# Kernel tuning notes

Hardware: AMD Instinct MI355X
Metric: run time of the kernel (lower is better)

The kernel has to match this reference:

```python
import jax, jax.numpy as jnp
import numpy as np

SELECTOR = jnp.array([29, 49, 79])
N_FINAL = 6
N_EM_ITERS = 10
LOG_2PI = float(np.log(2.0 * np.pi))


def _logdet2(c):
    # log determinant of trailing 2x2 matrices
    return jnp.log(c[..., 0, 0] * c[..., 1, 1] - c[..., 0, 1] * c[..., 1, 0])


def _inv2(c):
    # analytic inverse of trailing 2x2 matrices
    det = c[..., 0, 0] * c[..., 1, 1] - c[..., 0, 1] * c[..., 1, 0]
    inv = jnp.stack([
        jnp.stack([c[..., 1, 1], -c[..., 0, 1]], axis=-1),
        jnp.stack([-c[..., 1, 0], c[..., 0, 0]], axis=-1),
    ], axis=-2)
    return inv / det[..., None, None]


def _initial_state(probas, trajectories):
    B, M = probas.shape
    tsel = trajectories[:, :, SELECTOR, :]                       # [B,M,3,2]
    dots = jnp.einsum('bmtd,bntd->btmn', tsel, tsel)             # [B,3,M,M]
    d1 = jnp.einsum('bmtd,bmtd->btm', tsel, tsel)                # [B,3,M]
    R = jnp.sqrt(d1[:, :, :, None] + d1[:, :, None, :] - 2.0 * dots)
    thr = jnp.quantile(R[:, -1].reshape(B, -1), 0.15, axis=-1)[:, None, None, None]
    adj = (R <= thr).astype(probas.dtype).prod(axis=1)           # [B,M,M]
    worked = jnp.ones((B, M), dtype=probas.dtype)
    bidx = jnp.arange(B)
    idxs = []
    for _ in range(N_FINAL):
        score = (adj * probas[:, None, :]).sum(axis=2) * worked  # [B,M]
        amax = jnp.argmax(score, axis=-1)                        # [B]
        worked = worked * (1.0 - adj[bidx, amax])
        idxs.append(amax)
    return jnp.stack(idxs, axis=1)                               # [B,6]


def _coefficients(cov6, trajectories, traj6, probas6):
    cov6_sel = cov6[:, :, SELECTOR]                              # [B,6,3,2,2]
    prec = _inv2(cov6_sel)                                       # [B,6,3,2,2]
    diff = traj6[:, :, SELECTOR][:, :, None] - trajectories[:, :, SELECTOR][:, None]  # [B,6,M,3,2]
    qform = jnp.einsum('bnmti,bntij,bnmtj->bnmt', diff, prec, diff)
    logdet = _logdet2(cov6_sel)[:, :, None, :]                   # [B,6,1,3]
    pM = jnp.exp((-LOG_2PI - 0.5 * logdet - 0.5 * qform).sum(axis=-1)) + 1e-8  # [B,6,M]
    num = pM * probas6[:, :, None]
    return num / (num.sum(axis=1, keepdims=True) + 1e-8)


def _forward(non_normalized_probas, trajectories, covariance_matrices):
    B = trajectories.shape[0]
    probas = jax.nn.softmax(non_normalized_probas, axis=-1)
    idx = jax.lax.stop_gradient(_initial_state(probas, trajectories))  # [B,6]
    b = jnp.arange(B)[:, None]
    traj6 = trajectories[b, idx]                                 # [B,6,T,2]
    probas6 = jax.nn.softmax(jnp.take_along_axis(non_normalized_probas, idx, axis=1), axis=-1)
    cov6 = covariance_matrices[b, idx]                           # [B,6,T,2,2]
    for _ in range(N_EM_ITERS):
        pM = jax.lax.stop_gradient(_coefficients(cov6, trajectories, traj6, probas6))
        P = probas[:, None, :] * pM                              # [B,6,M]
        probas6 = P.sum(axis=-1)                                 # [B,6]
        traj6 = jnp.einsum('bnm,bmtd->bntd', P, trajectories) / probas6[:, :, None, None]
        diff = traj6[:, :, None] - trajectories[:, None]         # [B,6,M,T,2]
        cov6 = (jnp.einsum('bnm,bmtij->bntij', P, covariance_matrices)
                + jnp.einsum('bnm,bnmti,bnmtj->bntij', P, diff, diff)) / probas6[:, :, None, None, None]
    return probas6, traj6, cov6


def setup_inputs() -> dict:
    key = jax.random.key(0)
    k1, k2, k3 = jax.random.split(key, 3)
    B, M, T = 256, 48, 80
    logits = jax.random.normal(k1, (B, M), dtype=jnp.float32)
    trajectories = jax.random.normal(k2, (B, M, T, 2), dtype=jnp.float32)
    A = 0.3 * jax.random.normal(k3, (B, M, T, 2, 2), dtype=jnp.float32)
    cov = A @ jnp.swapaxes(A, -1, -2) + 0.5 * jnp.eye(2, dtype=jnp.float32)
    return {'non_normalized_probas': logits, 'trajectories': trajectories,
            'covariance_matrices': cov}


def reference(non_normalized_probas, trajectories, covariance_matrices):
    return _forward(non_normalized_probas, trajectories, covariance_matrices)
```

## Files before the change

### kernel.cpp

```cpp
#include <hip/hip_runtime.h>
#include <math.h>

#define BATCH 256
#define M 48
#define T 80
#define NF 6
#define EMIT 10
#define MM (M*M)
#define KPW 9
#define LOG2PI 1.8378770664093453f

typedef unsigned int u32;
typedef unsigned long long u64;

#define WGSYNC()     __asm__ __volatile__("s_waitcnt lgkmcnt(0)\ns_barrier" ::: "memory")
#define WGSYNC_ALL() __asm__ __volatile__("s_waitcnt vmcnt(0) lgkmcnt(0)\ns_barrier" ::: "memory")

__global__ __launch_bounds__(256, 1)
void em_kernel(const float* __restrict__ g_logits,
               const float* __restrict__ g_traj,
               const float* __restrict__ g_cov,
               float* __restrict__ g_out)
{
    const int b = blockIdx.x;
    const int tid = threadIdx.x;
    const int lane = tid & 63;
    const int wv = tid >> 6;
    const int SEL[3] = {29, 49, 79};

    __shared__ __align__(16) float s_txy[M*T*2];
    __shared__ __align__(16) float s_cv4[M*T*4];
    __shared__ float s_adj[MM];
    __shared__ float s_logits[M];
    __shared__ float s_probas[M];
    __shared__ float s_tsel[M*6];
    __shared__ float s_d1[M*3];
    __shared__ __align__(16) float s_csel[M*3*4];
    __shared__ __align__(16) float s_Pm[M*8];
    __shared__ float s_t6sel[2][NF*6];
    __shared__ float s_probas6[2][NF];
    __shared__ float s_prec[2][NF*3*3];
    __shared__ float s_ld[2][NF*3];
    __shared__ int   s_idx[8];
    __shared__ __align__(16) u32 s_hist[4][4][256];
    __shared__ u32 s_statc[4], s_statm[4];

    const float* traj_b = g_traj + (size_t)b*(M*T*2);
    const float* cov_b  = g_cov  + (size_t)b*(M*T*4);

    float myLogit = -1e30f;
    if (lane < M) myLogit = g_logits[b*M + lane];
    float selx[3], sely[3], cc0[3], cc1[3], cc2[3];
    #pragma unroll
    for (int r = 0; r < 3; ++r) {
        int i = lane + r*64;
        if (i < M*3) {
            int m = i/3, tt = i - (i/3)*3;
            float2 xy = ((const float2*)traj_b)[m*T + SEL[tt]];
            float4 cv = ((const float4*)cov_b)[m*T + SEL[tt]];
            selx[r]=xy.x; sely[r]=xy.y; cc0[r]=cv.x; cc1[r]=cv.y; cc2[r]=cv.w;
        }
    }

    __builtin_amdgcn_sched_barrier(0);
    {
        const char* gt = (const char*)traj_b + lane*16;
        char* lt = (char*)s_txy;
        #pragma unroll 2
        for (int k = wv; k < 30; k += 4)
            __builtin_amdgcn_global_load_lds(
                (const __attribute__((address_space(1))) u32*)(gt + k*1024),
                (__attribute__((address_space(3))) u32*)(lt + k*1024), 16, 0, 0);
        const char* gc = (const char*)cov_b + lane*16;
        char* lc = (char*)s_cv4;
        #pragma unroll 2
        for (int k = wv; k < 60; k += 4)
            __builtin_amdgcn_global_load_lds(
                (const __attribute__((address_space(1))) u32*)(gc + k*1024),
                (__attribute__((address_space(3))) u32*)(lc + k*1024), 16, 0, 0);
    }
    __builtin_amdgcn_sched_barrier(0);

    {
        uint4* hz = (uint4*)&s_hist[wv][0][0];
        #pragma unroll
        for (int k = 0; k < 4; ++k) hz[lane + k*64] = make_uint4(0,0,0,0);
    }

    if (lane < M) s_logits[lane] = myLogit;
    #pragma unroll
    for (int r = 0; r < 3; ++r) {
        int i = lane + r*64;
        if (i < M*3) {
            int m = i/3, tt = i - (i/3)*3;
            s_tsel[m*6+tt*2+0] = selx[r];
            s_tsel[m*6+tt*2+1] = sely[r];
            s_d1[i] = selx[r]*selx[r] + sely[r]*sely[r];
            s_csel[i*4+0]=cc0[r]; s_csel[i*4+1]=cc1[r]; s_csel[i*4+2]=cc2[r]; s_csel[i*4+3]=0.f;
        }
    }

    float mx = myLogit;
    #pragma unroll
    for (int off = 32; off; off >>= 1) mx = fmaxf(mx, __shfl_xor(mx, off));
    float pe = (lane < M) ? __expf(myLogit - mx) : 0.f;
    float psum = pe;
    #pragma unroll
    for (int off = 32; off; off >>= 1) psum += __shfl_xor(psum, off);
    const float proba = pe / psum;
    if (lane < M) s_probas[lane] = proba;

    u32 key[KPW];
    {
        u32* h0 = &s_hist[wv][0][0];
        #pragma unroll
        for (int j = 0; j < KPW; ++j) {
            int e = lane + (wv*KPW + j)*64;
            int m = e/M, n = e - (e/M)*M;
            float dot = s_tsel[m*6+4]*s_tsel[n*6+4] + s_tsel[m*6+5]*s_tsel[n*6+5];
            float v = s_d1[m*3+2] + s_d1[n*3+2] - 2.0f*dot;
            key[j] = __float_as_uint(fmaxf(v, 0.0f));
            atomicAdd(&h0[key[j] >> 24], 1u);
        }
    }

    int target = 345;
    u32 prefix = 0u, pmask = 0u;
    #pragma unroll 1
    for (int r = 0; r < 4; ++r) {
        const int shift = 24 - 8*r;
        if (r) {
            u32* hr = &s_hist[wv][r][0];
            #pragma unroll
            for (int j = 0; j < KPW; ++j) {
                if ((key[j] & pmask) == prefix)
                    atomicAdd(&hr[(key[j] >> shift) & 255u], 1u);
            }
        }
        WGSYNC();
        uint4 h0 = ((const uint4*)&s_hist[0][r][0])[lane];
        uint4 h1 = ((const uint4*)&s_hist[1][r][0])[lane];
        uint4 h2 = ((const uint4*)&s_hist[2][r][0])[lane];
        uint4 h3 = ((const uint4*)&s_hist[3][r][0])[lane];
        uint4 hv = make_uint4(h0.x+h1.x+h2.x+h3.x, h0.y+h1.y+h2.y+h3.y,
                              h0.z+h1.z+h2.z+h3.z, h0.w+h1.w+h2.w+h3.w);
        u32 s4 = hv.x + hv.y + hv.z + hv.w;
        u32 cum = s4;
        #pragma unroll
        for (int off = 1; off < 64; off <<= 1) {
            u32 u = __shfl_up(cum, off);
            if (lane >= off) cum += u;
        }
        u64 bmask = __ballot(cum > (u32)target);
        int g = __builtin_ctzll(bmask);
        int dig = 0; u32 binstart = 0;
        if (lane == g) {
            u32 exc = cum - s4;
            int bi2 = lane*4;
            if (exc + hv.x > (u32)target)      { dig = bi2;   binstart = exc; }
            else { exc += hv.x;
                if (exc + hv.y > (u32)target)  { dig = bi2+1; binstart = exc; }
                else { exc += hv.y;
                    if (exc + hv.z > (u32)target) { dig = bi2+2; binstart = exc; }
                    else { exc += hv.z;            dig = bi2+3; binstart = exc; } } }
        }
        dig = __shfl(dig, g);
        binstart = (u32)__shfl((int)binstart, g);
        target -= (int)binstart;
        prefix |= ((u32)dig) << shift;
        pmask  |= (255u << shift);
    }
    const u32 k1 = prefix;
    const float v1f = sqrtf(__uint_as_float(k1));

    {
        u32 cnt = 0, mng = 0xFFFFFFFFu;
        #pragma unroll
        for (int j = 0; j < KPW; ++j) {
            if (key[j] <= k1) cnt++;
            else mng = (key[j] < mng) ? key[j] : mng;
        }
        #pragma unroll
        for (int off = 32; off > 0; off >>= 1) {
            cnt += __shfl_down(cnt, off);
            u32 mo = (u32)__shfl_down((int)mng, off);
            mng = (mo < mng) ? mo : mng;
        }
        if (lane == 0) { s_statc[wv] = cnt; s_statm[wv] = mng; }
    }
    WGSYNC();
    float v2f;
    {
        u32 ct = s_statc[0]+s_statc[1]+s_statc[2]+s_statc[3];
        u32 mt = s_statm[0];
        if (s_statm[1] < mt) mt = s_statm[1];
        if (s_statm[2] < mt) mt = s_statm[2];
        if (s_statm[3] < mt) mt = s_statm[3];
        v2f = (ct >= 347u) ? v1f : sqrtf(__uint_as_float(mt));
    }
    const float qi = 0.15f * 2303.0f;
    const float fr = qi - floorf(qi);
    const float thr = v1f*(1.0f - fr) + v2f*fr;

    float dthr;
    {
        u32 ub = __float_as_uint(thr*thr);
        while (sqrtf(__uint_as_float(ub)) > thr) --ub;
        while (sqrtf(__uint_as_float(ub+1u)) <= thr) ++ub;
        dthr = __uint_as_float(ub);
    }

    #pragma unroll
    for (int j = 0; j < KPW; ++j) {
        int e = lane + (wv*KPW + j)*64;
        int m = e/M, n = e - (e/M)*M;
        float d0 = s_tsel[m*6+0]*s_tsel[n*6+0] + s_tsel[m*6+1]*s_tsel[n*6+1];
        float v0 = fmaxf(s_d1[m*3+0] + s_d1[n*3+0] - 2.0f*d0, 0.0f);
        float d1v = s_tsel[m*6+2]*s_tsel[n*6+2] + s_tsel[m*6+3]*s_tsel[n*6+3];
        float v1 = fmaxf(s_d1[m*3+1] + s_d1[n*3+1] - 2.0f*d1v, 0.0f);
        bool a = (__uint_as_float(key[j]) <= dthr) && (v0 <= dthr) && (v1 <= dthr);
        s_adj[e] = a ? 1.0f : 0.0f;
    }
    WGSYNC();

    const int m = (lane < M) ? lane : (M-1);
    {
        float base = 0.f;
        #pragma unroll
        for (int n = 0; n < M; ++n) base += s_adj[n*M+m] * s_probas[n];
        float worked = 1.f;
        #pragma unroll 1
        for (int k = 0; k < NF; ++k) {
            float sc = (lane < M) ? base*worked : -1.f;
            int bi = lane;
            #pragma unroll
            for (int off = 32; off; off >>= 1) {
                float so = __shfl_down(sc, off);
                int io = __shfl_down(bi, off);
                if (so > sc || (so == sc && io < bi)) { sc = so; bi = io; }
            }
            int amax = __shfl(bi, 0);
            if (lane == 0) s_idx[k] = amax;
            worked *= (1.f - s_adj[amax*M+m]);
        }
    }

    if (lane < NF) {
        float mx6 = -1e30f;
        #pragma unroll
        for (int j = 0; j < NF; ++j) mx6 = fmaxf(mx6, s_logits[s_idx[j]]);
        float sum6 = 0.f;
        #pragma unroll
        for (int j = 0; j < NF; ++j) sum6 += __expf(s_logits[s_idx[j]] - mx6);
        s_probas6[0][lane] = __expf(s_logits[s_idx[lane]] - mx6) / sum6;
    }
    if (lane < NF*3) {
        int n = lane/3, tt = lane - (lane/3)*3;
        int m0 = s_idx[n];
        s_t6sel[0][n*6+tt*2+0] = s_tsel[m0*6+tt*2+0];
        s_t6sel[0][n*6+tt*2+1] = s_tsel[m0*6+tt*2+1];
        float c00 = s_csel[(m0*3+tt)*4+0];
        float c01 = s_csel[(m0*3+tt)*4+1];
        float c11 = s_csel[(m0*3+tt)*4+2];
        float det = c00*c11 - c01*c01;
        float rdet = __fdividef(1.0f, det);
        s_prec[0][lane*3+0] =  c11*rdet;
        s_prec[0][lane*3+1] = -c01*rdet;
        s_prec[0][lane*3+2] =  c00*rdet;
        s_ld[0][lane] = __logf(det);
    }

    float tm0=s_tsel[m*6+0], tm1=s_tsel[m*6+1], tm2=s_tsel[m*6+2],
          tm3=s_tsel[m*6+3], tm4=s_tsel[m*6+4], tm5=s_tsel[m*6+5];
    const int gid = tid >> 3;
    const int sub = tid & 7;
    const int gn  = gid/3, gtt = gid - (gid/3)*3;
    const int gslot = (gn < 3) ? gn : gn + 1;

    #pragma unroll 1
    for (int it = 0; it < EMIT; ++it) {
        const int cur = it & 1, nxt = cur ^ 1;
        const float* prC = s_prec[cur];
        const float* ldC = s_ld[cur];
        const float* t6C = s_t6sel[cur];
        const float* p6C = s_probas6[cur];

        float num[NF]; float den = 1e-8f;
        #pragma unroll
        for (int n = 0; n < NF; ++n) {
            float lsum = ldC[n*3+0] + ldC[n*3+1] + ldC[n*3+2];
            float dx0 = t6C[n*6+0]-tm0, dy0 = t6C[n*6+1]-tm1;
            float dx1 = t6C[n*6+2]-tm2, dy1 = t6C[n*6+3]-tm3;
            float dx2 = t6C[n*6+4]-tm4, dy2 = t6C[n*6+5]-tm5;
            float q = prC[(n*3+0)*3+0]*dx0*dx0 + 2.f*prC[(n*3+0)*3+1]*dx0*dy0 + prC[(n*3+0)*3+2]*dy0*dy0
                    + prC[(n*3+1)*3+0]*dx1*dx1 + 2.f*prC[(n*3+1)*3+1]*dx1*dy1 + prC[(n*3+1)*3+2]*dy1*dy1
                    + prC[(n*3+2)*3+0]*dx2*dx2 + 2.f*prC[(n*3+2)*3+1]*dx2*dy2 + prC[(n*3+2)*3+2]*dy2*dy2;
            num[n] = (__expf(-3.f*LOG2PI - 0.5f*lsum - 0.5f*q) + 1e-8f) * p6C[n];
            den += num[n];
        }
        float f = __fdividef(proba, den);
        if (lane < M) {
            *(float4*)&s_Pm[m*8]   = make_float4(num[0]*f, num[1]*f, num[2]*f, 0.f);
            *(float4*)&s_Pm[m*8+4] = make_float4(num[3]*f, num[4]*f, num[5]*f, 0.f);
        }
        if (it == EMIT-1) break;

        if (gid < 18) {
            float SP=0,S1x=0,S1y=0,Sxx=0,Sxy=0,Syy=0,C0=0,C1=0,C2=0;
            #pragma unroll
            for (int k = 0; k < 6; ++k) {
                int mm = sub*6 + k;
                float p = s_Pm[mm*8 + gslot];
                float x = s_tsel[mm*6+gtt*2+0];
                float y = s_tsel[mm*6+gtt*2+1];
                float4 c4 = *(const float4*)&s_csel[(mm*3+gtt)*4];
                SP += p; S1x += p*x; S1y += p*y;
                Sxx += p*x*x; Sxy += p*x*y; Syy += p*y*y;
                C0 += p*c4.x; C1 += p*c4.y; C2 += p*c4.z;
            }
            #define R8(v) { v += __shfl_down(v,4); v += __shfl_down(v,2); v += __shfl_down(v,1); }
            R8(SP) R8(S1x) R8(S1y) R8(Sxx) R8(Sxy) R8(Syy) R8(C0) R8(C1) R8(C2)
            #undef R8
            if (sub == 0) {
                float p6 = SP;
                float tx = __fdividef(S1x, p6), ty = __fdividef(S1y, p6);
                float rp = __fdividef(1.0f, p6);
                float c00 = (C0 + (Sxx - S1x*tx)) * rp;
                float c01 = (C1 + (Sxy - S1x*ty)) * rp;
                float c11 = (C2 + (Syy - S1y*ty)) * rp;
                float det = c00*c11 - c01*c01;
                float rdet = __fdividef(1.0f, det);
                s_prec[nxt][gid*3+0] =  c11*rdet;
                s_prec[nxt][gid*3+1] = -c01*rdet;
                s_prec[nxt][gid*3+2] =  c00*rdet;
                s_ld[nxt][gid] = __logf(det);
                s_t6sel[nxt][gn*6+gtt*2+0] = tx;
                s_t6sel[nxt][gn*6+gtt*2+1] = ty;
                if (gtt == 0) s_probas6[nxt][gn] = SP;
            }
        }
        WGSYNC();
    }

    WGSYNC_ALL();

    float*  out_p = g_out;
    float2* out_t = (float2*)(g_out + BATCH*NF);
    float4* out_c = (float4*)(g_out + BATCH*NF + BATCH*NF*T*2);
    if (lane < 60) {
        int idx = wv*60 + lane;
        int t = idx/3, third = idx - (idx/3)*3;
        int nA = third*2, nB = nA + 1;
        int slotA = (nA < 3) ? nA : nA + 1;
        int slotB = (nB < 3) ? nB : nB + 1;
        float SPa=0,S1xa=0,S1ya=0,Sxxa=0,Sxya=0,Syya=0,C00a=0,C01a=0,C11a=0;
        float SPb=0,S1xb=0,S1yb=0,Sxxb=0,Sxyb=0,Syyb=0,C00b=0,C01b=0,C11b=0;
        #pragma unroll 4
        for (int mm = 0; mm < M; ++mm) {
            float2 xy = ((const float2*)s_txy)[mm*T + t];
            float4 c4 = ((const float4*)s_cv4)[mm*T + t];
            float pa = s_Pm[mm*8 + slotA];
            float pb = s_Pm[mm*8 + slotB];
            float xx = xy.x*xy.x, xyv = xy.x*xy.y, yy = xy.y*xy.y;
            SPa+=pa; S1xa+=pa*xy.x; S1ya+=pa*xy.y;
            Sxxa+=pa*xx; Sxya+=pa*xyv; Syya+=pa*yy;
            C00a+=pa*c4.x; C01a+=pa*c4.y; C11a+=pa*c4.w;
            SPb+=pb; S1xb+=pb*xy.x; S1yb+=pb*xy.y;
            Sxxb+=pb*xx; Sxyb+=pb*xyv; Syyb+=pb*yy;
            C00b+=pb*c4.x; C01b+=pb*c4.y; C11b+=pb*c4.w;
        }
        {
            float p6 = SPa;
            float tx = __fdividef(S1xa, p6), ty = __fdividef(S1ya, p6);
            float rp = __fdividef(1.0f, p6);
            float c00 = (C00a + (Sxxa - S1xa*tx)) * rp;
            float c01 = (C01a + (Sxya - S1xa*ty)) * rp;
            float c11 = (C11a + (Syya - S1ya*ty)) * rp;
            size_t o = (size_t)(b*NF + nA)*T + t;
            out_t[o] = make_float2(tx, ty);
            out_c[o] = make_float4(c00, c01, c01, c11);
        }
        {
            float p6 = SPb;
            float tx = __fdividef(S1xb, p6), ty = __fdividef(S1yb, p6);
            float rp = __fdividef(1.0f, p6);
            float c00 = (C00b + (Sxxb - S1xb*tx)) * rp;
            float c01 = (C01b + (Sxyb - S1xb*ty)) * rp;
            float c11 = (C11b + (Syyb - S1yb*ty)) * rp;
            size_t o = (size_t)(b*NF + nB)*T + t;
            out_t[o] = make_float2(tx, ty);
            out_c[o] = make_float4(c00, c01, c01, c11);
        }
    }
    if (wv == 0 && lane < NF) {
        int slot = (lane < 3) ? lane : lane + 1;
        float sp = 0.f;
        for (int mm = 0; mm < M; ++mm) sp += s_Pm[mm*8 + slot];
        out_p[b*NF + lane] = sp;
    }
}

extern "C" void kernel_launch(void* const* d_in, const int* in_sizes, int n_in,
                              void* d_out, int out_size, void* d_ws, size_t ws_size,
                              hipStream_t stream) {
    const float* logits = (const float*)d_in[0];
    const float* traj   = (const float*)d_in[1];
    const float* cov    = (const float*)d_in[2];
    float* out = (float*)d_out;
    em_kernel<<<dim3(BATCH), dim3(256), 0, stream>>>(logits, traj, cov, out);
}
```

Before: 105.4 us.

## Double workgroup to 512 threads and pack precision/mean state into vector LDS slots

Launches each batch element's workgroup with 512 threads instead of 256, spreading the pairwise-distance keys, histogram radix select and final M-step reduction over 8 waves with one output (t,n) per thread. Also packs precision entries and log-determinant into one float4 and the selected means into float2 so the E-step reads fewer, wider LDS loads. The aim is shorter per-block serial work. In exchange it adds more barrier participants and histogram merging across 8 waves, and some EM-loop code paths not shown may still assume 4 waves.

```diff
diff --git a/kernel.cpp b/kernel.cpp
--- a/kernel.cpp
+++ b/kernel.cpp
@@ -7,7 +7,7 @@
 #define NF 6
 #define EMIT 10
 #define MM (M*M)
-#define KPW 9
+#define NW 8
 #define LOG2PI 1.8378770664093453f
 
 typedef unsigned int u32;
@@ -16,7 +16,7 @@
 #define WGSYNC()     __asm__ __volatile__("s_waitcnt lgkmcnt(0)\ns_barrier" ::: "memory")
 #define WGSYNC_ALL() __asm__ __volatile__("s_waitcnt vmcnt(0) lgkmcnt(0)\ns_barrier" ::: "memory")
 
-__global__ __launch_bounds__(256, 1)
+__global__ __launch_bounds__(512, 1)
 void em_kernel(const float* __restrict__ g_logits,
                const float* __restrict__ g_traj,
                const float* __restrict__ g_cov,
@@ -37,13 +37,12 @@
     __shared__ float s_d1[M*3];
     __shared__ __align__(16) float s_csel[M*3*4];
     __shared__ __align__(16) float s_Pm[M*8];
-    __shared__ float s_t6sel[2][NF*6];
+    __shared__ __align__(16) float4 s_st[2][NF*3];
+    __shared__ __align__(8)  float2 s_t6[2][NF*3];
     __shared__ float s_probas6[2][NF];
-    __shared__ float s_prec[2][NF*3*3];
-    __shared__ float s_ld[2][NF*3];
     __shared__ int   s_idx[8];
-    __shared__ __align__(16) u32 s_hist[4][4][256];
-    __shared__ u32 s_statc[4], s_statm[4];
+    __shared__ __align__(16) u32 s_hist[NW][4][256];
+    __shared__ u32 s_statc[NW], s_statm[NW];
 
     const float* traj_b = g_traj + (size_t)b*(M*T*2);
     const float* cov_b  = g_cov  + (size_t)b*(M*T*4);
@@ -67,14 +66,14 @@
         const char* gt = (const char*)traj_b + lane*16;
         char* lt = (char*)s_txy;
         #pragma unroll 2
-        for (int k = wv; k < 30; k += 4)
+        for (int k = wv; k < 30; k += NW)
             __builtin_amdgcn_global_load_lds(
                 (const __attribute__((address_space(1))) u32*)(gt + k*1024),
                 (__attribute__((address_space(3))) u32*)(lt + k*1024), 16, 0, 0);
         const char* gc = (const char*)cov_b + lane*16;
         char* lc = (char*)s_cv4;
         #pragma unroll 2
-        for (int k = wv; k < 60; k += 4)
+        for (int k = wv; k < 60; k += NW)
             __builtin_amdgcn_global_load_lds(
                 (const __attribute__((address_space(1))) u32*)(gc + k*1024),
                 (__attribute__((address_space(3))) u32*)(lc + k*1024), 16, 0, 0);
@@ -110,12 +109,14 @@
     const float proba = pe / psum;
     if (lane < M) s_probas[lane] = proba;
 
-    u32 key[KPW];
+    const bool v5 = (tid < MM - 4*512);
+    u32 key[5];
     {
         u32* h0 = &s_hist[wv][0][0];
         #pragma unroll
-        for (int j = 0; j < KPW; ++j) {
-            int e = lane + (wv*KPW + j)*64;
+        for (int j = 0; j < 5; ++j) {
+            if (j == 4 && !v5) { key[j] = 0xFFFFFFFFu; continue; }
+            int e = tid + j*512;
             int m = e/M, n = e - (e/M)*M;
             float dot = s_tsel[m*6+4]*s_tsel[n*6+4] + s_tsel[m*6+5]*s_tsel[n*6+5];
             float v = s_d1[m*3+2] + s_d1[n*3+2] - 2.0f*dot;
@@ -132,18 +133,20 @@
         if (r) {
             u32* hr = &s_hist[wv][r][0];
             #pragma unroll
-            for (int j = 0; j < KPW; ++j) {
+            for (int j = 0; j < 5; ++j) {
+                if (j == 4 && !v5) continue;
                 if ((key[j] & pmask) == prefix)
                     atomicAdd(&hr[(key[j] >> shift) & 255u], 1u);
             }
         }
         WGSYNC();
-        uint4 h0 = ((const uint4*)&s_hist[0][r][0])[lane];
-        uint4 h1 = ((const uint4*)&s_hist[1][r][0])[lane];
-        uint4 h2 = ((const uint4*)&s_hist[2][r][0])[lane];
-        uint4 h3 = ((const uint4*)&s_hist[3][r][0])[lane];
-        uint4 hv = make_uint4(h0.x+h1.x+h2.x+h3.x, h0.y+h1.y+h2.y+h3.y,
-                              h0.z+h1.z+h2.z+h3.z, h0.w+h1.w+h2.w+h3.w);
+        u32 hx=0, hy=0, hz=0, hw=0;
+        #pragma unroll
+        for (int w = 0; w < NW; ++w) {
+            uint4 h = ((const uint4*)&s_hist[w][r][0])[lane];
+            hx += h.x; hy += h.y; hz += h.z; hw += h.w;
+        }
+        uint4 hv = make_uint4(hx, hy, hz, hw);
         u32 s4 = hv.x + hv.y + hv.z + hv.w;
         u32 cum = s4;
         #pragma unroll
@@ -176,7 +179,8 @@
     {
         u32 cnt = 0, mng = 0xFFFFFFFFu;
         #pragma unroll
-        for (int j = 0; j < KPW; ++j) {
+        for (int j = 0; j < 5; ++j) {
+            if (j == 4 && !v5) continue;
             if (key[j] <= k1) cnt++;
             else mng = (key[j] < mng) ? key[j] : mng;
         }
@@ -191,11 +195,12 @@
     WGSYNC();
     float v2f;
     {
-        u32 ct = s_statc[0]+s_statc[1]+s_statc[2]+s_statc[3];
-        u32 mt = s_statm[0];
-        if (s_statm[1] < mt) mt = s_statm[1];
-        if (s_statm[2] < mt) mt = s_statm[2];
-        if (s_statm[3] < mt) mt = s_statm[3];
+        u32 ct = 0, mt = 0xFFFFFFFFu;
+        #pragma unroll
+        for (int w = 0; w < NW; ++w) {
+            ct += s_statc[w];
+            if (s_statm[w] < mt) mt = s_statm[w];
+        }
         v2f = (ct >= 347u) ? v1f : sqrtf(__uint_as_float(mt));
     }
     const float qi = 0.15f * 2303.0f;
@@ -211,8 +216,9 @@
     }
 
     #pragma unroll
-    for (int j = 0; j < KPW; ++j) {
-        int e = lane + (wv*KPW + j)*64;
+    for (int j = 0; j < 5; ++j) {
+        if (j == 4 && !v5) continue;
+        int e = tid + j*512;
         int m = e/M, n = e - (e/M)*M;
         float d0 = s_tsel[m*6+0]*s_tsel[n*6+0] + s_tsel[m*6+1]*s_tsel[n*6+1];
         float v0 = fmaxf(s_d1[m*3+0] + s_d1[n*3+0] - 2.0f*d0, 0.0f);
@@ -257,17 +263,13 @@
     if (lane < NF*3) {
         int n = lane/3, tt = lane - (lane/3)*3;
         int m0 = s_idx[n];
-        s_t6sel[0][n*6+tt*2+0] = s_tsel[m0*6+tt*2+0];
-        s_t6sel[0][n*6+tt*2+1] = s_tsel[m0*6+tt*2+1];
+        s_t6[0][lane] = make_float2(s_tsel[m0*6+tt*2+0], s_tsel[m0*6+tt*2+1]);
         float c00 = s_csel[(m0*3+tt)*4+0];
         float c01 = s_csel[(m0*3+tt)*4+1];
         float c11 = s_csel[(m0*3+tt)*4+2];
         float det = c00*c11 - c01*c01;
         float rdet = __fdividef(1.0f, det);
-        s_prec[0][lane*3+0] =  c11*rdet;
-        s_prec[0][lane*3+1] = -c01*rdet;
-        s_prec[0][lane*3+2] =  c00*rdet;
-        s_ld[0][lane] = __logf(det);
+        s_st[0][lane] = make_float4(c11*rdet, -c01*rdet, c00*rdet, __logf(det));
     }
 
     float tm0=s_tsel[m*6+0], tm1=s_tsel[m*6+1], tm2=s_tsel[m*6+2],
@@ -280,21 +282,22 @@
     #pragma unroll 1
     for (int it = 0; it < EMIT; ++it) {
         const int cur = it & 1, nxt = cur ^ 1;
-        const float* prC = s_prec[cur];
-        const float* ldC = s_ld[cur];
-        const float* t6C = s_t6sel[cur];
-        const float* p6C = s_probas6[cur];
+        const float4* stC = s_st[cur];
+        const float2* t6C = s_t6[cur];
+        const float*  p6C = s_probas6[cur];
 
         float num[NF]; float den = 1e-8f;
         #pragma unroll
         for (int n = 0; n < NF; ++n) {
-            float lsum = ldC[n*3+0] + ldC[n*3+1] + ldC[n*3+2];
-            float dx0 = t6C[n*6+0]-tm0, dy0 = t6C[n*6+1]-tm1;
-            float dx1 = t6C[n*6+2]-tm2, dy1 = t6C[n*6+3]-tm3;
-            float dx2 = t6C[n*6+4]-tm4, dy2 = t6C[n*6+5]-tm5;
-            float q = prC[(n*3+0)*3+0]*dx0*dx0 + 2.f*prC[(n*3+0)*3+1]*dx0*dy0 + prC[(n*3+0)*3+2]*dy0*dy0
-                    + prC[(n*3+1)*3+0]*dx1*dx1 + 2.f*prC[(n*3+1)*3+1]*dx1*dy1 + prC[(n*3+1)*3+2]*dy1*dy1
-                    + prC[(n*3+2)*3+0]*dx2*dx2 + 2.f*prC[(n*3+2)*3+1]*dx2*dy2 + prC[(n*3+2)*3+2]*dy2*dy2;
+            float4 p0 = stC[n*3+0], p1 = stC[n*3+1], p2 = stC[n*3+2];
+            float2 a0 = t6C[n*3+0], a1 = t6C[n*3+1], a2 = t6C[n*3+2];
+            float lsum = p0.w + p1.w + p2.w;
+            float dx0 = a0.x-tm0, dy0 = a0.y-tm1;
+            float dx1 = a1.x-tm2, dy1 = a1.y-tm3;
+            float dx2 = a2.x-tm4, dy2 = a2.y-tm5;
+            float q = p0.x*dx0*dx0 + 2.f*p0.y*dx0*dy0 + p0.z*dy0*dy0
+                    + p1.x*dx1*dx1 + 2.f*p1.y*dx1*dy1 + p1.z*dy1*dy1
+                    + p2.x*dx2*dx2 + 2.f*p2.y*dx2*dy2 + p2.z*dy2*dy2;
             num[n] = (__expf(-3.f*LOG2PI - 0.5f*lsum - 0.5f*q) + 1e-8f) * p6C[n];
             den += num[n];
         }
@@ -330,12 +333,8 @@
                 float c11 = (C2 + (Syy - S1y*ty)) * rp;
                 float det = c00*c11 - c01*c01;
                 float rdet = __fdividef(1.0f, det);
-                s_prec[nxt][gid*3+0] =  c11*rdet;
-                s_prec[nxt][gid*3+1] = -c01*rdet;
-                s_prec[nxt][gid*3+2] =  c00*rdet;
-                s_ld[nxt][gid] = __logf(det);
-                s_t6sel[nxt][gn*6+gtt*2+0] = tx;
-                s_t6sel[nxt][gn*6+gtt*2+1] = ty;
+                s_st[nxt][gid] = make_float4(c11*rdet, -c01*rdet, c00*rdet, __logf(det));
+                s_t6[nxt][gid] = make_float2(tx, ty);
                 if (gtt == 0) s_probas6[nxt][gn] = SP;
             }
         }
@@ -347,50 +346,28 @@
     float*  out_p = g_out;
     float2* out_t = (float2*)(g_out + BATCH*NF);
     float4* out_c = (float4*)(g_out + BATCH*NF + BATCH*NF*T*2);
-    if (lane < 60) {
-        int idx = wv*60 + lane;
-        int t = idx/3, third = idx - (idx/3)*3;
-        int nA = third*2, nB = nA + 1;
-        int slotA = (nA < 3) ? nA : nA + 1;
-        int slotB = (nB < 3) ? nB : nB + 1;
-        float SPa=0,S1xa=0,S1ya=0,Sxxa=0,Sxya=0,Syya=0,C00a=0,C01a=0,C11a=0;
-        float SPb=0,S1xb=0,S1yb=0,Sxxb=0,Sxyb=0,Syyb=0,C00b=0,C01b=0,C11b=0;
+    if (tid < T*NF) {
+        int t = tid / NF, n = tid - (tid/NF)*NF;
+        int slot = (n < 3) ? n : n + 1;
+        float SP=0,S1x=0,S1y=0,Sxx=0,Sxy=0,Syy=0,C00=0,C01=0,C11=0;
         #pragma unroll 4
         for (int mm = 0; mm < M; ++mm) {
             float2 xy = ((const float2*)s_txy)[mm*T + t];
             float4 c4 = ((const float4*)s_cv4)[mm*T + t];
-            float pa = s_Pm[mm*8 + slotA];
-            float pb = s_Pm[mm*8 + slotB];
-            float xx = xy.x*xy.x, xyv = xy.x*xy.y, yy = xy.y*xy.y;
-            SPa+=pa; S1xa+=pa*xy.x; S1ya+=pa*xy.y;
-            Sxxa+=pa*xx; Sxya+=pa*xyv; Syya+=pa*yy;
-            C00a+=pa*c4.x; C01a+=pa*c4.y; C11a+=pa*c4.w;
-            SPb+=pb; S1xb+=pb*xy.x; S1yb+=pb*xy.y;
-            Sxxb+=pb*xx; Sxyb+=pb*xyv; Syyb+=pb*yy;
-            C00b+=pb*c4.x; C01b+=pb*c4.y; C11b+=pb*c4.w;
-        }
-        {
-            float p6 = SPa;
-            float tx = __fdividef(S1xa, p6), ty = __fdividef(S1ya, p6);
-            float rp = __fdividef(1.0f, p6);
-            float c00 = (C00a + (Sxxa - S1xa*tx)) * rp;
-            float c01 = (C01a + (Sxya - S1xa*ty)) * rp;
-            float c11 = (C11a + (Syya - S1ya*ty)) * rp;
-            size_t o = (size_t)(b*NF + nA)*T + t;
-            out_t[o] = make_float2(tx, ty);
-            out_c[o] = make_float4(c00, c01, c01, c11);
-        }
-        {
-            float p6 = SPb;
-            float tx = __fdividef(S1xb, p6), ty = __fdividef(S1yb, p6);
-            float rp = __fdividef(1.0f, p6);
-            float c00 = (C00b + (Sxxb - S1xb*tx)) * rp;
-            float c01 = (C01b + (Sxyb - S1xb*ty)) * rp;
-            float c11 = (C11b + (Syyb - S1yb*ty)) * rp;
-            size_t o = (size_t)(b*NF + nB)*T + t;
-            out_t[o] = make_float2(tx, ty);
-            out_c[o] = make_float4(c00, c01, c01, c11);
-        }
+            float p  = s_Pm[mm*8 + slot];
+            SP  += p;        S1x += p*xy.x;      S1y += p*xy.y;
+            Sxx += p*xy.x*xy.x; Sxy += p*xy.x*xy.y; Syy += p*xy.y*xy.y;
+            C00 += p*c4.x;   C01 += p*c4.y;      C11 += p*c4.w;
+        }
+        float p6 = SP;
+        float tx = __fdividef(S1x, p6), ty = __fdividef(S1y, p6);
+        float rp = __fdividef(1.0f, p6);
+        float c00 = (C00 + (Sxx - S1x*tx)) * rp;
+        float c01 = (C01 + (Sxy - S1x*ty)) * rp;
+        float c11 = (C11 + (Syy - S1y*ty)) * rp;
+        size_t o = (size_t)(b*NF + n)*T + t;
+        out_t[o] = make_float2(tx, ty);
+        out_c[o] = make_float4(c00, c01, c01, c11);
     }
     if (wv == 0 && lane < NF) {
         int slot = (lane < 3) ? lane : lane + 1;
@@ -407,5 +384,5 @@
     const float* traj   = (const float*)d_in[1];
     const float* cov    = (const float*)d_in[2];
     float* out = (float*)d_out;
-    em_kernel<<<dim3(BATCH), dim3(256), 0, stream>>>(logits, traj, cov, out);
+    em_kernel<<<dim3(BATCH), dim3(512), 0, stream>>>(logits, traj, cov, out);
 }
```

After: 105.5 us. Within noise of the previous version (+0.1%).
